# Optimization experiments

Measured on AMD Instinct MI355X. Metric: run time of the kernel, lower is better.

The kernel has to match this reference:

```python
import jax, jax.numpy as jnp
import numpy as np

NA, NF, EA, EF, NG = 200000, 50000, 800000, 200000, 4096
D = 128
BN_EPS = 1e-5

def _bn(x, g, b):
    m = x.mean(axis=0)
    v = x.var(axis=0)
    return g * (x - m) * jax.lax.rsqrt(v + BN_EPS) + b

def _gine(x, src, dst, edge_emb, W1, b1, g1, be1, W2, b2):
    # message = relu(x_src + edge_emb); scatter-add to dst; (1+eps)*x with eps=0
    msg = jax.nn.relu(x[src] + edge_emb)
    agg = jax.ops.segment_sum(msg, dst, num_segments=x.shape[0])
    h = x + agg
    h = jax.nn.relu(_bn(h @ W1 + b1, g1, be1))
    return h @ W2 + b2

def _seg_mean(x, idx, n):
    s = jax.ops.segment_sum(x, idx, num_segments=n)
    c = jax.ops.segment_sum(jnp.ones((x.shape[0],), x.dtype), idx, num_segments=n)
    return s / jnp.maximum(c, 1.0)[:, None]

def setup_inputs() -> dict:
    key = jax.random.key(0)
    ks = jax.random.split(key, 40)
    def nrm(i, shape, scale=0.05):
        return (jax.random.normal(ks[i], shape, dtype=jnp.float32) * scale)
    inp = {
        'atom_x': jax.random.normal(ks[0], (NA, 101), dtype=jnp.float32),
        'fg_x': jax.random.normal(ks[1], (NF, 73), dtype=jnp.float32),
        'atom_edge_attr': jax.random.normal(ks[2], (EA, 11), dtype=jnp.float32),
        'fg_edge_attr': jax.random.normal(ks[3], (EF, 101), dtype=jnp.float32),
        'atom_emb_W': nrm(4, (101, D)), 'atom_emb_b': jnp.zeros((D,), jnp.float32),
        'fg_emb_W': nrm(5, (73, D)), 'fg_emb_b': jnp.zeros((D,), jnp.float32),
        'bond_W': nrm(6, (3, 11, D)), 'bond_b': jnp.zeros((3, D), jnp.float32),
        'ag_W1': nrm(7, (3, D, 2 * D)), 'ag_b1': jnp.zeros((3, 2 * D), jnp.float32),
        'ag_g1': jnp.ones((3, 2 * D), jnp.float32), 'ag_be1': jnp.zeros((3, 2 * D), jnp.float32),
        'ag_W2': nrm(8, (3, 2 * D, D)), 'ag_b2': jnp.zeros((3, D), jnp.float32),
        'abn_g': jnp.ones((3, D), jnp.float32), 'abn_b': jnp.zeros((3, D), jnp.float32),
        'fge_W': nrm(9, (2, 101, D)), 'fge_b': jnp.zeros((2, D), jnp.float32),
        'fg_W1': nrm(10, (2, D, 2 * D)), 'fg_b1': jnp.zeros((2, 2 * D), jnp.float32),
        'fg_g1': jnp.ones((2, 2 * D), jnp.float32), 'fg_be1': jnp.zeros((2, 2 * D), jnp.float32),
        'fg_W2': nrm(11, (2, 2 * D, D)), 'fg_b2': jnp.zeros((2, D), jnp.float32),
        'fbn_g': jnp.ones((2, D), jnp.float32), 'fbn_b': jnp.zeros((2, D), jnp.float32),
        'a2f_W': nrm(12, (D, D)), 'a2f_b': jnp.zeros((D,), jnp.float32),
        'atom_edge_index': jax.random.randint(ks[13], (2, EA), 0, NA, dtype=jnp.int32),
        'fg_edge_index': jax.random.randint(ks[14], (2, EF), 0, NF, dtype=jnp.int32),
        'atom_idx': jax.random.randint(ks[15], (NA,), 0, NA, dtype=jnp.int32),
        'fg_idx': jax.random.randint(ks[16], (NA,), 0, NF, dtype=jnp.int32),
        'fg_batch': jnp.sort(jax.random.randint(ks[17], (NF,), 0, NG, dtype=jnp.int32)),
    }
    return inp

def reference(atom_x, fg_x, atom_edge_attr, fg_edge_attr, atom_emb_W, atom_emb_b, fg_emb_W, fg_emb_b, bond_W, bond_b, ag_W1, ag_b1, ag_g1, ag_be1, ag_W2, ag_b2, abn_g, abn_b, fge_W, fge_b, fg_W1, fg_b1, fg_g1, fg_be1, fg_W2, fg_b2, fbn_g, fbn_b, a2f_W, a2f_b, atom_edge_index, fg_edge_index, atom_idx, fg_idx, fg_batch):
    asrc, adst = atom_edge_index[0], atom_edge_index[1]
    fsrc, fdst = fg_edge_index[0], fg_edge_index[1]
    h = atom_x @ atom_emb_W + atom_emb_b
    for i in range(3):
        eemb = atom_edge_attr @ bond_W[i] + bond_b[i]
        h = _gine(h, asrc, adst, eemb, ag_W1[i], ag_b1[i], ag_g1[i], ag_be1[i], ag_W2[i], ag_b2[i])
        h = _bn(h, abn_g[i], abn_b[i])
        if i != 2:
            h = jax.nn.relu(h)
    a2f = _seg_mean(h[atom_idx], fg_idx, NF) @ a2f_W + a2f_b
    g = fg_x @ fg_emb_W + fg_emb_b + a2f
    for i in range(2):
        eemb = fg_edge_attr @ fge_W[i] + fge_b[i]
        g = _gine(g, fsrc, fdst, eemb, fg_W1[i], fg_b1[i], fg_g1[i], fg_be1[i], fg_W2[i], fg_b2[i])
        g = _bn(g, fbn_g[i], fbn_b[i])
        if i != 1:
            g = jax.nn.relu(g)
    return _seg_mean(g, fg_batch, NG)
```

## Files before the change

### kernel.cpp

```cpp
#include <hip/hip_runtime.h>
#include <cstddef>
#include <cstdint>

#define NA_C 200000
#define NF_C 50000
#define EA_C 800000
#define EF_C 200000
#define NG_C 4096
#define DD 128
#define HH 256
#define SC_CHUNK 2048
#define NPW 8

typedef unsigned short u16;
typedef unsigned int   u32;
typedef float f32x4 __attribute__((ext_vector_type(4)));
typedef short s16x8 __attribute__((ext_vector_type(8)));

__device__ inline float bf2f(u16 h) { return __uint_as_float(((u32)h) << 16); }
__device__ inline u16 f2bf(float f) {
    u32 u = __float_as_uint(f);
    return (u16)((u + 0x7fffu + ((u >> 16) & 1u)) >> 16);
}
__device__ inline float2 up2(u32 u) {
    return make_float2(__uint_as_float(u << 16), __uint_as_float(u & 0xffff0000u));
}
__device__ inline u32 pk2(float x, float y) { return (u32)f2bf(x) | ((u32)f2bf(y) << 16); }

__global__ __launch_bounds__(256) void gemm_b(
    const u16* __restrict__ A, const u16* __restrict__ Bt,
    const float* __restrict__ bias,
    const float* __restrict__ iscale, const float* __restrict__ ishift,
    const u16* __restrict__ Cadd, u16* __restrict__ C,
    int M, int K, int Ntot,
    float* __restrict__ ssum, float* __restrict__ ssq)
{
    __shared__ u16 As[4 * 128 * 8];
    __shared__ u16 Bs[4 * 128 * 8];
    __shared__ float ls[128], lq[128];
    const int tid  = threadIdx.x;
    const int wave = tid >> 6, lane = tid & 63;
    const int quad = lane >> 4, l15 = lane & 15;
    const int wm = (wave & 1) * 64, wn = (wave >> 1) * 64;
    const int m0 = blockIdx.y * 128, n0 = blockIdx.x * 128;
    const int r     = tid >> 1;
    const int cpair = (tid & 1) * 2;

    f32x4 acc[4][4];
#pragma unroll
    for (int i = 0; i < 4; ++i)
#pragma unroll
        for (int j = 0; j < 4; ++j) acc[i][j] = (f32x4)0.f;

    const int m = m0 + r;
    for (int k0 = 0; k0 < K; k0 += 32) {
#pragma unroll
        for (int j = 0; j < 2; ++j) {
            const int cg = cpair + j;
            uint4 av = make_uint4(0, 0, 0, 0);
            if (m < M) av = *(const uint4*)(A + (size_t)m * K + k0 + cg * 8);
            if (iscale) {
                u32* w = (u32*)&av;
#pragma unroll
                for (int q2 = 0; q2 < 4; ++q2) {
                    int kk = k0 + cg * 8 + q2 * 2;
                    float2 f = up2(w[q2]);
                    f.x = fmaxf(fmaf(f.x, iscale[kk],     ishift[kk]),     0.f);
                    f.y = fmaxf(fmaf(f.y, iscale[kk + 1], ishift[kk + 1]), 0.f);
                    w[q2] = pk2(f.x, f.y);
                }
            }
            *(uint4*)&As[(cg * 128 + r) * 8] = av;
        }
#pragma unroll
        for (int j = 0; j < 2; ++j) {
            const int cg = cpair + j;
            uint4 bv = *(const uint4*)(Bt + (size_t)(n0 + r) * K + k0 + cg * 8);
            *(uint4*)&Bs[(cg * 128 + r) * 8] = bv;
        }
        __syncthreads();

        s16x8 a[4], b[4];
#pragma unroll
        for (int mi = 0; mi < 4; ++mi)
            a[mi] = *(const s16x8*)&As[(quad * 128 + wm + mi * 16 + l15) * 8];
#pragma unroll
        for (int ni = 0; ni < 4; ++ni)
            b[ni] = *(const s16x8*)&Bs[(quad * 128 + wn + ni * 16 + l15) * 8];
#pragma unroll
        for (int mi = 0; mi < 4; ++mi)
#pragma unroll
            for (int ni = 0; ni < 4; ++ni)
                acc[mi][ni] = __builtin_amdgcn_mfma_f32_16x16x32_bf16(
                    a[mi], b[ni], acc[mi][ni], 0, 0, 0);
        __syncthreads();
    }

    if (ssum) {
        if (tid < 128) { ls[tid] = 0.f; lq[tid] = 0.f; }
        __syncthreads();
    }

    float cs[4] = {0.f, 0.f, 0.f, 0.f}, cq[4] = {0.f, 0.f, 0.f, 0.f};
#pragma unroll
    for (int mi = 0; mi < 4; ++mi) {
        int rowb = m0 + wm + mi * 16 + quad * 4;
#pragma unroll
        for (int ni = 0; ni < 4; ++ni) {
            int col = n0 + wn + ni * 16 + l15;
            float bv = bias[col];
#pragma unroll
            for (int rr = 0; rr < 4; ++rr) {
                int row = rowb + rr;
                if (row < M) {
                    float v = acc[mi][ni][rr] + bv;
                    size_t idx = (size_t)row * Ntot + col;
                    if (Cadd) v += bf2f(Cadd[idx]);
                    C[idx] = f2bf(v);
                    cs[ni] += v;
                    cq[ni] = fmaf(v, v, cq[ni]);
                }
            }
        }
    }

    if (ssum) {
#pragma unroll
        for (int ni = 0; ni < 4; ++ni) {
            int lc = wn + ni * 16 + l15;
            atomicAdd(&ls[lc], cs[ni]);
            atomicAdd(&lq[lc], cq[ni]);
        }
        __syncthreads();
        if (tid < 128) {
            atomicAdd(&ssum[n0 + tid], ls[tid]);
            atomicAdd(&ssq[n0 + tid], lq[tid]);
        }
    }
}

static inline void gemm_launch(hipStream_t s, const u16* A, const u16* Bt,
    const float* bias, const float* iscale, const float* ishift,
    const u16* Cadd, u16* C, int M, int K, int Ntot,
    float* ssum = nullptr, float* ssq = nullptr)
{
    dim3 grid(Ntot / 128, (M + 127) / 128);
    gemm_b<<<grid, dim3(256), 0, s>>>(A, Bt, bias, iscale, ishift, Cadd, C,
                                      M, K, Ntot, ssum, ssq);
}

__global__ void cvt_pad(const float* __restrict__ src, u32* __restrict__ dst,
                        int M, int K, int Kp2)
{
    int idx = blockIdx.x * 256 + threadIdx.x;
    if (idx >= M * Kp2) return;
    int row = idx / Kp2, c = (idx - row * Kp2) * 2;
    float a = (c < K)     ? src[(size_t)row * K + c]     : 0.f;
    float b = (c + 1 < K) ? src[(size_t)row * K + c + 1] : 0.f;
    dst[idx] = pk2(a, b);
}

__global__ void cvt_pad_perm(const float* __restrict__ src, const int2* __restrict__ csr2,
                             u32* __restrict__ dst, int M, int K, int Kp2)
{
    int idx = blockIdx.x * 256 + threadIdx.x;
    if (idx >= M * Kp2) return;
    int row = idx / Kp2, c = (idx - row * Kp2) * 2;
    int srow = csr2[row].x;
    float a = (c < K)     ? src[(size_t)srow * K + c]     : 0.f;
    float b = (c + 1 < K) ? src[(size_t)srow * K + c + 1] : 0.f;
    dst[idx] = pk2(a, b);
}

__global__ void perm_attr12_k(const float* __restrict__ attr, const int2* __restrict__ csr2,
                              float* __restrict__ out, int ne)
{
    int idx = blockIdx.x * 256 + threadIdx.x;
    if (idx >= ne * 12) return;
    int e = idx / 12, k = idx - e * 12;
    int eid = csr2[e].x;
    out[idx] = (k < 11) ? attr[(size_t)eid * 11 + k] : 0.f;
}

__global__ void prep_wt(const float* __restrict__ W, u16* __restrict__ Wt,
                        int K, int N, int Kp)
{
    int idx = blockIdx.x * 256 + threadIdx.x;
    if (idx >= N * Kp) return;
    int n = idx / Kp, k = idx - n * Kp;
    Wt[idx] = (k < K) ? f2bf(W[(size_t)k * N + n]) : (u16)0;
}

__global__ void hist_k(const int* __restrict__ idx, int n, int* __restrict__ deg)
{
    int i = blockIdx.x * 256 + threadIdx.x;
    if (i < n) atomicAdd(&deg[idx[i]], 1);
}

__global__ __launch_bounds__(256) void scan_part_k(const int* __restrict__ deg, int n,
                                                   int* __restrict__ bsum)
{
    __shared__ int ts[256];
    const int t = threadIdx.x;
    const int base = blockIdx.x * SC_CHUNK + t * 8;
    int s = 0;
#pragma unroll
    for (int j = 0; j < 8; ++j) { int i = base + j; if (i < n) s += deg[i]; }
    ts[t] = s;
    __syncthreads();
    for (int off = 128; off > 0; off >>= 1) {
        if (t < off) ts[t] += ts[t + off];
        __syncthreads();
    }
    if (t == 0) bsum[blockIdx.x] = ts[0];
}

__global__ __launch_bounds__(256) void scan_top_k(int* __restrict__ bsum, int nb)
{
    __shared__ int ss[256];
    const int t = threadIdx.x;
    int v = (t < nb) ? bsum[t] : 0;
    ss[t] = v;
    __syncthreads();
    for (int off = 1; off < 256; off <<= 1) {
        int u = (t >= off) ? ss[t - off] : 0;
        __syncthreads();
        ss[t] += u;
        __syncthreads();
    }
    if (t < nb) bsum[t] = ss[t] - v;
}

__global__ __launch_bounds__(256) void scan_emit_k(const int* __restrict__ deg, int n,
                                                   const int* __restrict__ bsum,
                                                   int* __restrict__ rowptr)
{
    __shared__ int ts[256];
    const int t = threadIdx.x;
    const int base = blockIdx.x * SC_CHUNK + t * 8;
    int d[8], loc[8], s = 0;
#pragma unroll
    for (int j = 0; j < 8; ++j) {
        int i = base + j;
        d[j] = (i < n) ? deg[i] : 0;
        loc[j] = s;
        s += d[j];
    }
    ts[t] = s;
    __syncthreads();
    for (int off = 1; off < 256; off <<= 1) {
        int u = (t >= off) ? ts[t - off] : 0;
        __syncthreads();
        ts[t] += u;
        __syncthreads();
    }
    const int off0 = bsum[blockIdx.x] + (ts[t] - s);
#pragma unroll
    for (int j = 0; j < 8; ++j) {
        int i = base + j;
        if (i < n) {
            rowptr[i] = off0 + loc[j];
            if (i == n - 1) rowptr[n] = off0 + loc[j] + d[j];
        }
    }
}

static void csr_prefix(hipStream_t s, const int* idx, int ne, int nbkt,
                       int* rowptr, int* cursor, int* bsum)
{
    hipMemsetAsync(cursor, 0, (size_t)nbkt * 4, s);
    hist_k<<<(ne + 255) / 256, 256, 0, s>>>(idx, ne, cursor);
    int nblk = (nbkt + SC_CHUNK - 1) / SC_CHUNK;
    scan_part_k<<<nblk, 256, 0, s>>>(cursor, nbkt, bsum);
    scan_top_k<<<1, 256, 0, s>>>(bsum, nblk);
    scan_emit_k<<<nblk, 256, 0, s>>>(cursor, nbkt, bsum, rowptr);
    hipMemcpyAsync(cursor, rowptr, (size_t)nbkt * 4, hipMemcpyDeviceToDevice, s);
}

__global__ void fill2_k(const int* __restrict__ idx, const int* __restrict__ src,
                        int n, int* __restrict__ cursor, int2* __restrict__ csr2)
{
    int i = blockIdx.x * 256 + threadIdx.x;
    if (i < n) {
        int p = atomicAdd(&cursor[idx[i]], 1);
        csr2[p] = make_int2(i, src[i]);
    }
}

__global__ void fillm_k(const int* __restrict__ idx, const int* __restrict__ map,
                        int n, int* __restrict__ cursor, int* __restrict__ csr)
{
    int i = blockIdx.x * 256 + threadIdx.x;
    if (i < n) {
        int p = atomicAdd(&cursor[idx[i]], 1);
        csr[p] = map ? map[i] : i;
    }
}

__global__ __launch_bounds__(256) void gine_agg_atom_b(
    const u32* __restrict__ x2, const float4* __restrict__ attrp,
    const int2* __restrict__ csr2, const int* __restrict__ rowptr,
    const float* __restrict__ Wm, const float* __restrict__ bm,
    const float* __restrict__ tsc, const float* __restrict__ tsh, int trelu,
    u32* __restrict__ out2, int n)
{
    const int lane = threadIdx.x & 63;
    const int v0 = (blockIdx.x * 4 + (threadIdx.x >> 6)) * NPW;
    if (v0 >= n) return;
    const int vend = (v0 + NPW < n) ? v0 + NPW : n;

    const float2 w0 = *(const float2*)&Wm[0 * 128 + 2 * lane];
    const float2 w1 = *(const float2*)&Wm[1 * 128 + 2 * lane];
    const float2 w2 = *(const float2*)&Wm[2 * 128 + 2 * lane];
    const float2 w3 = *(const float2*)&Wm[3 * 128 + 2 * lane];
    const float2 w4 = *(const float2*)&Wm[4 * 128 + 2 * lane];
    const float2 w5 = *(const float2*)&Wm[5 * 128 + 2 * lane];
    const float2 w6 = *(const float2*)&Wm[6 * 128 + 2 * lane];
    const float2 w7 = *(const float2*)&Wm[7 * 128 + 2 * lane];
    const float2 w8 = *(const float2*)&Wm[8 * 128 + 2 * lane];
    const float2 w9 = *(const float2*)&Wm[9 * 128 + 2 * lane];
    const float2 wa = *(const float2*)&Wm[10 * 128 + 2 * lane];
    const float2 bb = *(const float2*)&bm[2 * lane];

    float sc0 = 1.f, sc1 = 1.f, sh0 = 0.f, sh1 = 0.f;
    if (tsc) {
        sc0 = tsc[2 * lane]; sc1 = tsc[2 * lane + 1];
        sh0 = tsh[2 * lane]; sh1 = tsh[2 * lane + 1];
    }

    const int E0 = rowptr[v0], E1 = rowptr[vend];
    int v  = v0;
    int nb = rowptr[v0 + 1];
    u32 xs_n = (v0 + 1 < vend) ? x2[(size_t)(v0 + 1) * 64 + lane] : 0u;
    float2 acc = up2(x2[(size_t)v0 * 64 + lane]);
    acc.x = fmaf(acc.x, sc0, sh0); acc.y = fmaf(acc.y, sc1, sh1);
    if (trelu) { acc.x = fmaxf(acc.x, 0.f); acc.y = fmaxf(acc.y, 0.f); }

    if (E0 < E1) {
        int2 pc = csr2[E0];
        int2 pn = csr2[(E0 + 1 < E1) ? E0 + 1 : E0];
        float4 a0c = attrp[3 * (size_t)E0];
        float4 a1c = attrp[3 * (size_t)E0 + 1];
        float4 a2c = attrp[3 * (size_t)E0 + 2];
        u32 xc = x2[(size_t)pc.y * 64 + lane];
        for (int e = E0; e < E1; ++e) {
            const int en  = (e + 1 < E1) ? e + 1 : e;
            const int en2 = (e + 2 < E1) ? e + 2 : en;
            int2 p2 = csr2[en2];
            u32 xn = x2[(size_t)pn.y * 64 + lane];
            float4 a0n = attrp[3 * (size_t)en];
            float4 a1n = attrp[3 * (size_t)en + 1];
            float4 a2n = attrp[3 * (size_t)en + 2];
            while (e >= nb) {
                out2[(size_t)v * 64 + lane] = pk2(acc.x, acc.y);
                ++v;
                float2 nx = up2(xs_n);
                nx.x = fmaf(nx.x, sc0, sh0); nx.y = fmaf(nx.y, sc1, sh1);
                if (trelu) { nx.x = fmaxf(nx.x, 0.f); nx.y = fmaxf(nx.y, 0.f); }
                acc = nx;
                xs_n = (v + 1 < vend) ? x2[(size_t)(v + 1) * 64 + lane] : xs_n;
                nb = rowptr[v + 1];
            }
            float m0 = bb.x, m1 = bb.y;
            m0 = fmaf(a0c.x, w0.x, m0); m1 = fmaf(a0c.x, w0.y, m1);
            m0 = fmaf(a0c.y, w1.x, m0); m1 = fmaf(a0c.y, w1.y, m1);
            m0 = fmaf(a0c.z, w2.x, m0); m1 = fmaf(a0c.z, w2.y, m1);
            m0 = fmaf(a0c.w, w3.x, m0); m1 = fmaf(a0c.w, w3.y, m1);
            m0 = fmaf(a1c.x, w4.x, m0); m1 = fmaf(a1c.x, w4.y, m1);
            m0 = fmaf(a1c.y, w5.x, m0); m1 = fmaf(a1c.y, w5.y, m1);
            m0 = fmaf(a1c.z, w6.x, m0); m1 = fmaf(a1c.z, w6.y, m1);
            m0 = fmaf(a1c.w, w7.x, m0); m1 = fmaf(a1c.w, w7.y, m1);
            m0 = fmaf(a2c.x, w8.x, m0); m1 = fmaf(a2c.x, w8.y, m1);
            m0 = fmaf(a2c.y, w9.x, m0); m1 = fmaf(a2c.y, w9.y, m1);
            m0 = fmaf(a2c.z, wa.x, m0); m1 = fmaf(a2c.z, wa.y, m1);
            float2 s = up2(xc);
            s.x = fmaf(s.x, sc0, sh0); s.y = fmaf(s.y, sc1, sh1);
            if (trelu) { s.x = fmaxf(s.x, 0.f); s.y = fmaxf(s.y, 0.f); }
            acc.x += fmaxf(s.x + m0, 0.f);
            acc.y += fmaxf(s.y + m1, 0.f);
            pn = p2; xc = xn;
            a0c = a0n; a1c = a1n; a2c = a2n;
        }
    }
    for (;;) {
        out2[(size_t)v * 64 + lane] = pk2(acc.x, acc.y);
        ++v;
        if (v >= vend) break;
        float2 nx = up2(xs_n);
        nx.x = fmaf(nx.x, sc0, sh0); nx.y = fmaf(nx.y, sc1, sh1);
        if (trelu) { nx.x = fmaxf(nx.x, 0.f); nx.y = fmaxf(nx.y, 0.f); }
        acc = nx;
        xs_n = (v + 1 < vend) ? x2[(size_t)(v + 1) * 64 + lane] : xs_n;
    }
}

__global__ __launch_bounds__(256) void gine_agg_pre_b(
    const u32* __restrict__ x2, const u32* __restrict__ eemb2,
    const int2* __restrict__ csr2, const int* __restrict__ rowptr,
    const float* __restrict__ tsc, const float* __restrict__ tsh, int trelu,
    u32* __restrict__ out2, int n)
{
    const int lane = threadIdx.x & 63;
    const int v0 = (blockIdx.x * 4 + (threadIdx.x >> 6)) * NPW;
    if (v0 >= n) return;
    const int vend = (v0 + NPW < n) ? v0 + NPW : n;

    float sc0 = 1.f, sc1 = 1.f, sh0 = 0.f, sh1 = 0.f;
    if (tsc) {
        sc0 = tsc[2 * lane]; sc1 = tsc[2 * lane + 1];
        sh0 = tsh[2 * lane]; sh1 = tsh[2 * lane + 1];
    }

    const int E0 = rowptr[v0], E1 = rowptr[vend];
    int v  = v0;
    int nb = rowptr[v0 + 1];
    u32 xs_n = (v0 + 1 < vend) ? x2[(size_t)(v0 + 1) * 64 + lane] : 0u;
    float2 acc = up2(x2[(size_t)v0 * 64 + lane]);
    acc.x = fmaf(acc.x, sc0, sh0); acc.y = fmaf(acc.y, sc1, sh1);
    if (trelu) { acc.x = fmaxf(acc.x, 0.f); acc.y = fmaxf(acc.y, 0.f); }

    if (E0 < E1) {
        int2 pc = csr2[E0];
        int2 pn = csr2[(E0 + 1 < E1) ? E0 + 1 : E0];
        u32 xc = x2[(size_t)pc.y * 64 + lane];
        u32 mc = eemb2[(size_t)E0 * 64 + lane];
        for (int e = E0; e < E1; ++e) {
            const int en  = (e + 1 < E1) ? e + 1 : e;
            const int en2 = (e + 2 < E1) ? e + 2 : en;
            int2 p2 = csr2[en2];
            u32 xn = x2[(size_t)pn.y * 64 + lane];
            u32 mn = eemb2[(size_t)en * 64 + lane];
            while (e >= nb) {
                out2[(size_t)v * 64 + lane] = pk2(acc.x, acc.y);
                ++v;
                float2 nx = up2(xs_n);
                nx.x = fmaf(nx.x, sc0, sh0); nx.y = fmaf(nx.y, sc1, sh1);
                if (trelu) { nx.x = fmaxf(nx.x, 0.f); nx.y = fmaxf(nx.y, 0.f); }
                acc = nx;
                xs_n = (v + 1 < vend) ? x2[(size_t)(v + 1) * 64 + lane] : xs_n;
                nb = rowptr[v + 1];
            }
            float2 m = up2(mc);
            float2 s = up2(xc);
            s.x = fmaf(s.x, sc0, sh0); s.y = fmaf(s.y, sc1, sh1);
            if (trelu) { s.x = fmaxf(s.x, 0.f); s.y = fmaxf(s.y, 0.f); }
            acc.x += fmaxf(m.x + s.x, 0.f);
            acc.y += fmaxf(m.y + s.y, 0.f);
            pn = p2; xc = xn; mc = mn;
        }
    }
    for (;;) {
        out2[(size_t)v * 64 + lane] = pk2(acc.x, acc.y);
        ++v;
        if (v >= vend) break;
        float2 nx = up2(xs_n);
        nx.x = fmaf(nx.x, sc0, sh0); nx.y = fmaf(nx.y, sc1, sh1);
        if (trelu) { nx.x = fmaxf(nx.x, 0.f); nx.y = fmaxf(nx.y, 0.f); }
        acc = nx;
        xs_n = (v + 1 < vend) ? x2[(size_t)(v + 1) * 64 + lane] : xs_n;
    }
}

__global__ __launch_bounds__(256) void seg_mean_b2b(
    const u32* __restrict__ x2, const int* __restrict__ csr,
    const int* __restrict__ rowptr,
    const float* __restrict__ tsc, const float* __restrict__ tsh,
    u32* __restrict__ out2, int n)
{
    const int lane = threadIdx.x & 63;
    const int v = blockIdx.x * 4 + (threadIdx.x >> 6);
    if (v >= n) return;
    const int e0 = rowptr[v], e1 = rowptr[v + 1];
    float2 acc = make_float2(0.f, 0.f);
    if (e0 < e1) {
        int cc = csr[e0];
        int cn = csr[(e0 + 1 < e1) ? e0 + 1 : e0];
        u32 xc = x2[(size_t)cc * 64 + lane];
        for (int e = e0; e < e1; ++e) {
            const int en  = (e + 1 < e1) ? e + 1 : e;
            const int en2 = (e + 2 < e1) ? e + 2 : en;
            int c2 = csr[en2];
            u32 xn = x2[(size_t)cn * 64 + lane];
            float2 s = up2(xc);
            acc.x += s.x; acc.y += s.y;
            cn = c2; xc = xn;
        }
    }
    float inv = 1.f / fmaxf((float)(e1 - e0), 1.f);
    float2 r = make_float2(acc.x * inv, acc.y * inv);
    if (tsc) {
        if (e1 > e0) {
            r.x = fmaf(r.x, tsc[2 * lane],     tsh[2 * lane]);
            r.y = fmaf(r.y, tsc[2 * lane + 1], tsh[2 * lane + 1]);
        } else {
            r.x = 0.f; r.y = 0.f;
        }
    }
    out2[(size_t)v * 64 + lane] = pk2(r.x, r.y);
}

__global__ __launch_bounds__(256) void seg_mean_b2f(
    const u32* __restrict__ x2, const int* __restrict__ csr,
    const int* __restrict__ rowptr,
    const float* __restrict__ tsc, const float* __restrict__ tsh,
    float* __restrict__ out, int n)
{
    const int lane = threadIdx.x & 63;
    const int v = blockIdx.x * 4 + (threadIdx.x >> 6);
    if (v >= n) return;
    const int e0 = rowptr[v], e1 = rowptr[v + 1];
    float2 acc = make_float2(0.f, 0.f);
    if (e0 < e1) {
        int cc = csr[e0];
        int cn = csr[(e0 + 1 < e1) ? e0 + 1 : e0];
        u32 xc = x2[(size_t)cc * 64 + lane];
        for (int e = e0; e < e1; ++e) {
            const int en  = (e + 1 < e1) ? e + 1 : e;
            const int en2 = (e + 2 < e1) ? e + 2 : en;
            int c2 = csr[en2];
            u32 xn = x2[(size_t)cn * 64 + lane];
            float2 s = up2(xc);
            acc.x += s.x; acc.y += s.y;
            cn = c2; xc = xn;
        }
    }
    float inv = 1.f / fmaxf((float)(e1 - e0), 1.f);
    float2 r = make_float2(acc.x * inv, acc.y * inv);
    if (tsc) {
        if (e1 > e0) {
            r.x = fmaf(r.x, tsc[2 * lane],     tsh[2 * lane]);
            r.y = fmaf(r.y, tsc[2 * lane + 1], tsh[2 * lane + 1]);
        } else {
            r.x = 0.f; r.y = 0.f;
        }
    }
    *(float2*)&out[(size_t)v * 128 + lane * 2] = r;
}

__global__ void bn_finalize(const float* __restrict__ sum, const float* __restrict__ sumsq,
                            const float* __restrict__ g, const float* __restrict__ be,
                            float minv, float* __restrict__ sc, float* __restrict__ sh, int N)
{
    int c = threadIdx.x;
    if (c < N) {
        float m = sum[c] * minv;
        float v = fmaxf(sumsq[c] * minv - m * m, 0.f);
        float s = g[c] * rsqrtf(v + 1e-5f);
        sc[c] = s;
        sh[c] = fmaf(-m, s, be[c]);
    }
}

extern "C" void kernel_launch(void* const* d_in, const int* in_sizes, int n_in,
                              void* d_out, int out_size, void* d_ws, size_t ws_size,
                              hipStream_t stream)
{
    const float* atom_x        = (const float*)d_in[0];
    const float* fg_x          = (const float*)d_in[1];
    const float* atom_edge_attr= (const float*)d_in[2];
    const float* fg_edge_attr  = (const float*)d_in[3];
    const float* atom_emb_W    = (const float*)d_in[4];
    const float* atom_emb_b    = (const float*)d_in[5];
    const float* fg_emb_W      = (const float*)d_in[6];
    const float* fg_emb_b      = (const float*)d_in[7];
    const float* bond_W        = (const float*)d_in[8];
    const float* bond_b        = (const float*)d_in[9];
    const float* ag_W1         = (const float*)d_in[10];
    const float* ag_b1         = (const float*)d_in[11];
    const float* ag_g1         = (const float*)d_in[12];
    const float* ag_be1        = (const float*)d_in[13];
    const float* ag_W2         = (const float*)d_in[14];
    const float* ag_b2         = (const float*)d_in[15];
    const float* abn_g         = (const float*)d_in[16];
    const float* abn_b         = (const float*)d_in[17];
    const float* fge_W         = (const float*)d_in[18];
    const float* fge_b         = (const float*)d_in[19];
    const float* fg_W1         = (const float*)d_in[20];
    const float* fg_b1         = (const float*)d_in[21];
    const float* fg_g1         = (const float*)d_in[22];
    const float* fg_be1        = (const float*)d_in[23];
    const float* fg_W2         = (const float*)d_in[24];
    const float* fg_b2         = (const float*)d_in[25];
    const float* fbn_g         = (const float*)d_in[26];
    const float* fbn_b         = (const float*)d_in[27];
    const float* a2f_W         = (const float*)d_in[28];
    const float* a2f_b         = (const float*)d_in[29];
    const int*   aei           = (const int*)d_in[30];
    const int*   fei           = (const int*)d_in[31];
    const int*   atom_idx      = (const int*)d_in[32];
    const int*   fg_idx        = (const int*)d_in[33];
    const int*   fg_batch      = (const int*)d_in[34];
    const int *asrc = aei, *adst = aei + EA_C;
    const int *fsrc = fei, *fdst = fei + EF_C;

    char* base = (char*)d_ws;
    const size_t SZ_H = (size_t)NA_C * DD * 2;
    u16* hA = (u16*)base;
    u16* hB = (u16*)(base + SZ_H);
    u16* TB = (u16*)(base + 2 * SZ_H);
    u16* XB = (u16*)(base + 2 * SZ_H + (size_t)NA_C * HH * 2);
    char* csrb = (char*)XB + SZ_H;
    int*  aR  = (int*)csrb;
    int*  aCu = aR + (NA_C + 2);
    int*  bS  = aCu + NA_C;
    int2* aE2 = (int2*)(bS + 258);
    char* wtb = (char*)(aE2 + EA_C);
    wtb = (char*)(((uintptr_t)wtb + 15) & ~(uintptr_t)15);
    u16* WT_aemb = (u16*)wtb;                 wtb += 128 * 128 * 2;
    u16* WT_aW1  = (u16*)wtb;                 wtb += 3 * 256 * 128 * 2;
    u16* WT_aW2  = (u16*)wtb;                 wtb += 3 * 128 * 256 * 2;
    u16* WT_a2f  = (u16*)wtb;                 wtb += 128 * 128 * 2;
    u16* WT_femb = (u16*)wtb;                 wtb += 128 * 96 * 2;
    u16* WT_fge  = (u16*)wtb;                 wtb += 2 * 128 * 128 * 2;
    u16* WT_fW1  = (u16*)wtb;                 wtb += 2 * 256 * 128 * 2;
    u16* WT_fW2  = (u16*)wtb;                 wtb += 2 * 128 * 256 * 2;
    float* stats = (float*)wtb;               wtb += 10240 * sizeof(float);
    float* S_SUM = stats;
    float* S_SQ  = stats + 2560;
    float* S_SC  = stats + 5120;
    float* S_SH  = stats + 7680;

    {
        int g = (128 * 128 + 255) / 256;
        prep_wt<<<g, 256, 0, stream>>>(atom_emb_W, WT_aemb, 101, 128, 128);
        prep_wt<<<g, 256, 0, stream>>>(a2f_W, WT_a2f, 128, 128, 128);
        for (int i = 0; i < 3; ++i) {
            prep_wt<<<(256 * 128 + 255) / 256, 256, 0, stream>>>(
                ag_W1 + (size_t)i * 128 * 256, WT_aW1 + (size_t)i * 256 * 128, 128, 256, 128);
            prep_wt<<<(128 * 256 + 255) / 256, 256, 0, stream>>>(
                ag_W2 + (size_t)i * 256 * 128, WT_aW2 + (size_t)i * 128 * 256, 256, 128, 256);
        }
        prep_wt<<<(128 * 96 + 255) / 256, 256, 0, stream>>>(fg_emb_W, WT_femb, 73, 128, 96);
        for (int i = 0; i < 2; ++i) {
            prep_wt<<<g, 256, 0, stream>>>(
                fge_W + (size_t)i * 101 * 128, WT_fge + (size_t)i * 128 * 128, 101, 128, 128);
            prep_wt<<<(256 * 128 + 255) / 256, 256, 0, stream>>>(
                fg_W1 + (size_t)i * 128 * 256, WT_fW1 + (size_t)i * 256 * 128, 128, 256, 128);
            prep_wt<<<(128 * 256 + 255) / 256, 256, 0, stream>>>(
                fg_W2 + (size_t)i * 256 * 128, WT_fW2 + (size_t)i * 128 * 256, 256, 128, 256);
        }
    }
    hipMemsetAsync(stats, 0, 5120 * sizeof(float), stream);

    csr_prefix(stream, adst, EA_C, NA_C, aR, aCu, bS);
    fill2_k<<<(EA_C + 255) / 256, 256, 0, stream>>>(adst, asrc, EA_C, aCu, aE2);

    cvt_pad<<<((size_t)NA_C * 64 + 255) / 256, 256, 0, stream>>>(atom_x, (u32*)XB, NA_C, 101, 64);

    gemm_launch(stream, XB, WT_aemb, atom_emb_b, nullptr, nullptr, nullptr, hA, NA_C, 128, 128);

    float* attrP = (float*)XB;
    perm_attr12_k<<<((size_t)EA_C * 12 + 255) / 256, 256, 0, stream>>>(
        atom_edge_attr, aE2, attrP, EA_C);

    const int agrid = (NA_C + 4 * NPW - 1) / (4 * NPW);
    u16* hc = hA;
    const float* cur_sc = nullptr;
    const float* cur_sh = nullptr;
    int cur_relu = 0;
    for (int i = 0; i < 3; ++i) {
        u16* hn = (hc == hA) ? hB : hA;
        const int st1 = 2 * i, st2 = 2 * i + 1;
        gine_agg_atom_b<<<agrid, 256, 0, stream>>>(
            (const u32*)hc, (const float4*)attrP, aE2, aR,
            bond_W + (size_t)i * 11 * DD, bond_b + i * DD,
            cur_sc, cur_sh, cur_relu, (u32*)hn, NA_C);
        gemm_launch(stream, hn, WT_aW1 + (size_t)i * 256 * 128,
                    ag_b1 + i * HH, nullptr, nullptr, nullptr, TB, NA_C, 128, HH,
                    S_SUM + st1 * 256, S_SQ + st1 * 256);
        bn_finalize<<<1, HH, 0, stream>>>(S_SUM + st1 * 256, S_SQ + st1 * 256,
                                          ag_g1 + i * HH, ag_be1 + i * HH,
                                          1.f / NA_C, S_SC + st1 * 256, S_SH + st1 * 256, HH);
        gemm_launch(stream, TB, WT_aW2 + (size_t)i * 128 * 256,
                    ag_b2 + i * DD, S_SC + st1 * 256, S_SH + st1 * 256, nullptr, hn,
                    NA_C, 256, 128,
                    S_SUM + st2 * 256, S_SQ + st2 * 256);
        bn_finalize<<<1, DD, 0, stream>>>(S_SUM + st2 * 256, S_SQ + st2 * 256,
                                          abn_g + i * DD, abn_b + i * DD,
                                          1.f / NA_C, S_SC + st2 * 256, S_SH + st2 * 256, DD);
        cur_sc = S_SC + st2 * 256; cur_sh = S_SH + st2 * 256; cur_relu = (i != 2);
        hc = hn;
    }

    {
        int* xE = (int*)aE2;
        csr_prefix(stream, fg_idx, NA_C, NF_C, aR, aCu, bS);
        fillm_k<<<(NA_C + 255) / 256, 256, 0, stream>>>(fg_idx, atom_idx, NA_C, aCu, xE);
        seg_mean_b2b<<<(NF_C + 3) / 4, 256, 0, stream>>>(
            (const u32*)hc, xE, aR, cur_sc, cur_sh, (u32*)hA, NF_C);
    }
    u16* means   = hA;
    u16* a2f_lin = hA + (size_t)NF_C * DD;
    gemm_launch(stream, means, WT_a2f, a2f_b, nullptr, nullptr, nullptr, a2f_lin, NF_C, 128, 128);

    u16* fgx_bf = hA + (size_t)NF_C * DD * 2;
    cvt_pad<<<((size_t)NF_C * 48 + 255) / 256, 256, 0, stream>>>(fg_x, (u32*)fgx_bf, NF_C, 73, 48);
    u16* g = hB;
    gemm_launch(stream, fgx_bf, WT_femb, fg_emb_b, nullptr, nullptr, a2f_lin, g, NF_C, 96, 128);

    csr_prefix(stream, fdst, EF_C, NF_C, aR, aCu, bS);
    fill2_k<<<(EF_C + 255) / 256, 256, 0, stream>>>(fdst, fsrc, EF_C, aCu, aE2);
    cvt_pad_perm<<<((size_t)EF_C * 64 + 255) / 256, 256, 0, stream>>>(
        fg_edge_attr, aE2, (u32*)XB, EF_C, 101, 64);

    const int fgrid = (NF_C + 4 * NPW - 1) / (4 * NPW);
    u16* eemb = TB;
    u16* gn   = hA + (size_t)NF_C * DD * 2 + (size_t)NF_C * 96;
    u16* gt   = TB + (size_t)EF_C * DD;
    const float* gsc = nullptr;
    const float* gsh = nullptr;
    int grelu = 0;
    for (int i = 0; i < 2; ++i) {
        const int st1 = 6 + 2 * i, st2 = 7 + 2 * i;
        gemm_launch(stream, XB, WT_fge + (size_t)i * 128 * 128,
                    fge_b + i * DD, nullptr, nullptr, nullptr, eemb, EF_C, 128, 128);
        gine_agg_pre_b<<<fgrid, 256, 0, stream>>>(
            (const u32*)g, (const u32*)eemb, aE2, aR, gsc, gsh, grelu, (u32*)gn, NF_C);
        gemm_launch(stream, gn, WT_fW1 + (size_t)i * 256 * 128,
                    fg_b1 + i * HH, nullptr, nullptr, nullptr, gt, NF_C, 128, HH,
                    S_SUM + st1 * 256, S_SQ + st1 * 256);
        bn_finalize<<<1, HH, 0, stream>>>(S_SUM + st1 * 256, S_SQ + st1 * 256,
                                          fg_g1 + i * HH, fg_be1 + i * HH,
                                          1.f / NF_C, S_SC + st1 * 256, S_SH + st1 * 256, HH);
        gemm_launch(stream, gt, WT_fW2 + (size_t)i * 128 * 256,
                    fg_b2 + i * DD, S_SC + st1 * 256, S_SH + st1 * 256, nullptr, g,
                    NF_C, 256, 128,
                    S_SUM + st2 * 256, S_SQ + st2 * 256);
        bn_finalize<<<1, DD, 0, stream>>>(S_SUM + st2 * 256, S_SQ + st2 * 256,
                                          fbn_g + i * DD, fbn_b + i * DD,
                                          1.f / NF_C, S_SC + st2 * 256, S_SH + st2 * 256, DD);
        gsc = S_SC + st2 * 256; gsh = S_SH + st2 * 256; grelu = (i != 1);
    }

    {
        int* bR  = (int*)(gt + (size_t)NF_C * HH);
        int* bCu = bR + (NG_C + 1);
        int* bE  = bCu + NG_C;
        csr_prefix(stream, fg_batch, NF_C, NG_C, bR, bCu, bS);
        fillm_k<<<(NF_C + 255) / 256, 256, 0, stream>>>(fg_batch, nullptr, NF_C, bCu, bE);
        seg_mean_b2f<<<(NG_C + 3) / 4, 256, 0, stream>>>(
            (const u32*)g, bE, bR, gsc, gsh, (float*)d_out, NG_C);
    }
}
```

Before: 2.173 ms.

## Fuse BN finalize into consumers, batch weight prep, use direct-to-LDS GEMM loads

Removes the standalone bn_finalize kernels. Each consumer (GEMM prologue, aggregation kernels, segment-mean kernels) now computes the BN scale and shift from the raw sum and sum-of-squares buffers. The fifteen prep_wt launches become a single job-table kernel, which cuts per-launch overhead. The GEMM's unscaled A path and its B loads now use global_load_lds to copy 16 bytes straight into LDS instead of staging through registers. The A path drops the row bounds check, so the last partial tile reads past M rows, which relies on the buffer extending that far.

```diff
diff --git a/kernel.cpp b/kernel.cpp
--- a/kernel.cpp
+++ b/kernel.cpp
@@ -27,10 +27,17 @@
 }
 __device__ inline u32 pk2(float x, float y) { return (u32)f2bf(x) | ((u32)f2bf(y) << 16); }
 
+__device__ inline void gll16(const void* g, void* l) {
+    __builtin_amdgcn_global_load_lds(
+        (const __attribute__((address_space(1))) void*)g,
+        (__attribute__((address_space(3))) void*)l, 16, 0, 0);
+}
+
 __global__ __launch_bounds__(256) void gemm_b(
     const u16* __restrict__ A, const u16* __restrict__ Bt,
     const float* __restrict__ bias,
-    const float* __restrict__ iscale, const float* __restrict__ ishift,
+    const float* __restrict__ isum, const float* __restrict__ isq,
+    const float* __restrict__ ig, const float* __restrict__ ibe, float iminv,
     const u16* __restrict__ Cadd, u16* __restrict__ C,
     int M, int K, int Ntot,
     float* __restrict__ ssum, float* __restrict__ ssq)
@@ -38,6 +45,7 @@
     __shared__ u16 As[4 * 128 * 8];
     __shared__ u16 Bs[4 * 128 * 8];
     __shared__ float ls[128], lq[128];
+    __shared__ float sIsc[256], sIsh[256];
     const int tid  = threadIdx.x;
     const int wave = tid >> 6, lane = tid & 63;
     const int quad = lane >> 4, l15 = lane & 15;
@@ -46,6 +54,17 @@
     const int r     = tid >> 1;
     const int cpair = (tid & 1) * 2;
 
+    if (isum) {
+        if (tid < K) {
+            float mu = isum[tid] * iminv;
+            float va = fmaxf(isq[tid] * iminv - mu * mu, 0.f);
+            float s  = ig[tid] * rsqrtf(va + 1e-5f);
+            sIsc[tid] = s;
+            sIsh[tid] = fmaf(-mu, s, ibe[tid]);
+        }
+        __syncthreads();
+    }
+
     f32x4 acc[4][4];
 #pragma unroll
     for (int i = 0; i < 4; ++i)
@@ -54,29 +73,34 @@
 
     const int m = m0 + r;
     for (int k0 = 0; k0 < K; k0 += 32) {
-#pragma unroll
-        for (int j = 0; j < 2; ++j) {
-            const int cg = cpair + j;
-            uint4 av = make_uint4(0, 0, 0, 0);
-            if (m < M) av = *(const uint4*)(A + (size_t)m * K + k0 + cg * 8);
-            if (iscale) {
+        if (isum) {
+#pragma unroll
+            for (int j = 0; j < 2; ++j) {
+                const int cg = cpair + j;
+                uint4 av = make_uint4(0, 0, 0, 0);
+                if (m < M) av = *(const uint4*)(A + (size_t)m * K + k0 + cg * 8);
                 u32* w = (u32*)&av;
 #pragma unroll
                 for (int q2 = 0; q2 < 4; ++q2) {
                     int kk = k0 + cg * 8 + q2 * 2;
                     float2 f = up2(w[q2]);
-                    f.x = fmaxf(fmaf(f.x, iscale[kk],     ishift[kk]),     0.f);
-                    f.y = fmaxf(fmaf(f.y, iscale[kk + 1], ishift[kk + 1]), 0.f);
+                    f.x = fmaxf(fmaf(f.x, sIsc[kk],     sIsh[kk]),     0.f);
+                    f.y = fmaxf(fmaf(f.y, sIsc[kk + 1], sIsh[kk + 1]), 0.f);
                     w[q2] = pk2(f.x, f.y);
                 }
+                *(uint4*)&As[(cg * 128 + r) * 8] = av;
             }
-            *(uint4*)&As[(cg * 128 + r) * 8] = av;
+        } else {
+#pragma unroll
+            for (int j = 0; j < 2; ++j) {
+                gll16(A + (size_t)(m0 + j * 64 + lane) * K + k0 + wave * 8,
+                      &As[(wave * 128 + j * 64) * 8]);
+            }
         }
 #pragma unroll
         for (int j = 0; j < 2; ++j) {
-            const int cg = cpair + j;
-            uint4 bv = *(const uint4*)(Bt + (size_t)(n0 + r) * K + k0 + cg * 8);
-            *(uint4*)&Bs[(cg * 128 + r) * 8] = bv;
+            gll16(Bt + (size_t)(n0 + j * 64 + lane) * K + k0 + wave * 8,
+                  &Bs[(wave * 128 + j * 64) * 8]);
         }
         __syncthreads();
 
@@ -140,13 +164,14 @@
 }
 
 static inline void gemm_launch(hipStream_t s, const u16* A, const u16* Bt,
-    const float* bias, const float* iscale, const float* ishift,
-    const u16* Cadd, u16* C, int M, int K, int Ntot,
+    const float* bias,
+    const float* isum, const float* isq, const float* ig, const float* ibe,
+    float iminv, const u16* Cadd, u16* C, int M, int K, int Ntot,
     float* ssum = nullptr, float* ssq = nullptr)
 {
     dim3 grid(Ntot / 128, (M + 127) / 128);
-    gemm_b<<<grid, dim3(256), 0, s>>>(A, Bt, bias, iscale, ishift, Cadd, C,
-                                      M, K, Ntot, ssum, ssq);
+    gemm_b<<<grid, dim3(256), 0, s>>>(A, Bt, bias, isum, isq, ig, ibe, iminv,
+                                      Cadd, C, M, K, Ntot, ssum, ssq);
 }
 
 __global__ void cvt_pad(const float* __restrict__ src, u32* __restrict__ dst,
@@ -182,13 +207,25 @@
     out[idx] = (k < 11) ? attr[(size_t)eid * 11 + k] : 0.f;
 }
 
-__global__ void prep_wt(const float* __restrict__ W, u16* __restrict__ Wt,
-                        int K, int N, int Kp)
+#define NJOBS 15
+struct WtJobs {
+    const float* W[NJOBS];
+    u16* Wt[NJOBS];
+    int K[NJOBS], N[NJOBS], Kp[NJOBS], end[NJOBS];
+};
+
+__global__ void prep_wt_all(WtJobs jobs, int total)
 {
     int idx = blockIdx.x * 256 + threadIdx.x;
-    if (idx >= N * Kp) return;
-    int n = idx / Kp, k = idx - n * Kp;
-    Wt[idx] = (k < K) ? f2bf(W[(size_t)k * N + n]) : (u16)0;
+    if (idx >= total) return;
+    int j = 0;
+    while (idx >= jobs.end[j]) ++j;
+    int base = j ? jobs.end[j - 1] : 0;
+    int loc = idx - base;
+    int Kp = jobs.Kp[j];
+    int n = loc / Kp, k = loc - n * Kp;
+    jobs.Wt[j][loc] = (k < jobs.K[j])
+        ? f2bf(jobs.W[j][(size_t)k * jobs.N[j] + n]) : (u16)0;
 }
 
 __global__ void hist_k(const int* __restrict__ idx, int n, int* __restrict__ deg)
@@ -297,11 +334,26 @@
     }
 }
 
+__device__ inline void bn_lane(const float* bsum, const float* bsq,
+                               const float* bg, const float* bbe, float minv,
+                               int lane, float& sc0, float& sc1, float& sh0, float& sh1)
+{
+    float mu0 = bsum[2 * lane] * minv,     mu1 = bsum[2 * lane + 1] * minv;
+    float va0 = fmaxf(bsq[2 * lane] * minv - mu0 * mu0, 0.f);
+    float va1 = fmaxf(bsq[2 * lane + 1] * minv - mu1 * mu1, 0.f);
+    sc0 = bg[2 * lane] * rsqrtf(va0 + 1e-5f);
+    sc1 = bg[2 * lane + 1] * rsqrtf(va1 + 1e-5f);
+    sh0 = fmaf(-mu0, sc0, bbe[2 * lane]);
+    sh1 = fmaf(-mu1, sc1, bbe[2 * lane + 1]);
+}
+
 __global__ __launch_bounds__(256) void gine_agg_atom_b(
     const u32* __restrict__ x2, const float4* __restrict__ attrp,
     const int2* __restrict__ csr2, const int* __restrict__ rowptr,
     const float* __restrict__ Wm, const float* __restrict__ bm,
-    const float* __restrict__ tsc, const float* __restrict__ tsh, int trelu,
+    const float* __restrict__ bsum, const float* __restrict__ bsq,
+    const float* __restrict__ bg, const float* __restrict__ bbe,
+    float bminv, int trelu,
     u32* __restrict__ out2, int n)
 {
     const int lane = threadIdx.x & 63;
@@ -323,10 +375,7 @@
     const float2 bb = *(const float2*)&bm[2 * lane];
 
     float sc0 = 1.f, sc1 = 1.f, sh0 = 0.f, sh1 = 0.f;
-    if (tsc) {
-        sc0 = tsc[2 * lane]; sc1 = tsc[2 * lane + 1];
-        sh0 = tsh[2 * lane]; sh1 = tsh[2 * lane + 1];
-    }
+    if (bsum) bn_lane(bsum, bsq, bg, bbe, bminv, lane, sc0, sc1, sh0, sh1);
 
     const int E0 = rowptr[v0], E1 = rowptr[vend];
     int v  = v0;
@@ -397,7 +446,9 @@
 __global__ __launch_bounds__(256) void gine_agg_pre_b(
     const u32* __restrict__ x2, const u32* __restrict__ eemb2,
     const int2* __restrict__ csr2, const int* __restrict__ rowptr,
-    const float* __restrict__ tsc, const float* __restrict__ tsh, int trelu,
+    const float* __restrict__ bsum, const float* __restrict__ bsq,
+    const float* __restrict__ bg, const float* __restrict__ bbe,
+    float bminv, int trelu,
     u32* __restrict__ out2, int n)
 {
     const int lane = threadIdx.x & 63;
@@ -406,10 +457,7 @@
     const int vend = (v0 + NPW < n) ? v0 + NPW : n;
 
     float sc0 = 1.f, sc1 = 1.f, sh0 = 0.f, sh1 = 0.f;
-    if (tsc) {
-        sc0 = tsc[2 * lane]; sc1 = tsc[2 * lane + 1];
-        sh0 = tsh[2 * lane]; sh1 = tsh[2 * lane + 1];
-    }
+    if (bsum) bn_lane(bsum, bsq, bg, bbe, bminv, lane, sc0, sc1, sh0, sh1);
 
     const int E0 = rowptr[v0], E1 = rowptr[vend];
     int v  = v0;
@@ -464,7 +512,8 @@
 __global__ __launch_bounds__(256) void seg_mean_b2b(
     const u32* __restrict__ x2, const int* __restrict__ csr,
     const int* __restrict__ rowptr,
-    const float* __restrict__ tsc, const float* __restrict__ tsh,
+    const float* __restrict__ bsum, const float* __restrict__ bsq,
+    const float* __restrict__ bg, const float* __restrict__ bbe, float bminv,
     u32* __restrict__ out2, int n)
 {
     const int lane = threadIdx.x & 63;
@@ -488,10 +537,12 @@
     }
     float inv = 1.f / fmaxf((float)(e1 - e0), 1.f);
     float2 r = make_float2(acc.x * inv, acc.y * inv);
-    if (tsc) {
+    if (bsum) {
         if (e1 > e0) {
-            r.x = fmaf(r.x, tsc[2 * lane],     tsh[2 * lane]);
-            r.y = fmaf(r.y, tsc[2 * lane + 1], tsh[2 * lane + 1]);
+            float sc0, sc1, sh0, sh1;
+            bn_lane(bsum, bsq, bg, bbe, bminv, lane, sc0, sc1, sh0, sh1);
+            r.x = fmaf(r.x, sc0, sh0);
+            r.y = fmaf(r.y, sc1, sh1);
         } else {
             r.x = 0.f; r.y = 0.f;
         }
@@ -502,7 +553,8 @@
 __global__ __launch_bounds__(256) void seg_mean_b2f(
     const u32* __restrict__ x2, const int* __restrict__ csr,
     const int* __restrict__ rowptr,
-    const float* __restrict__ tsc, const float* __restrict__ tsh,
+    const float* __restrict__ bsum, const float* __restrict__ bsq,
+    const float* __restrict__ bg, const float* __restrict__ bbe, float bminv,
     float* __restrict__ out, int n)
 {
     const int lane = threadIdx.x & 63;
@@ -526,29 +578,17 @@
     }
     float inv = 1.f / fmaxf((float)(e1 - e0), 1.f);
     float2 r = make_float2(acc.x * inv, acc.y * inv);
-    if (tsc) {
+    if (bsum) {
         if (e1 > e0) {
-            r.x = fmaf(r.x, tsc[2 * lane],     tsh[2 * lane]);
-            r.y = fmaf(r.y, tsc[2 * lane + 1], tsh[2 * lane + 1]);
+            float sc0, sc1, sh0, sh1;
+            bn_lane(bsum, bsq, bg, bbe, bminv, lane, sc0, sc1, sh0, sh1);
+            r.x = fmaf(r.x, sc0, sh0);
+            r.y = fmaf(r.y, sc1, sh1);
         } else {
             r.x = 0.f; r.y = 0.f;
         }
     }
     *(float2*)&out[(size_t)v * 128 + lane * 2] = r;
-}
-
-__global__ void bn_finalize(const float* __restrict__ sum, const float* __restrict__ sumsq,
-                            const float* __restrict__ g, const float* __restrict__ be,
-                            float minv, float* __restrict__ sc, float* __restrict__ sh, int N)
-{
-    int c = threadIdx.x;
-    if (c < N) {
-        float m = sum[c] * minv;
-        float v = fmaxf(sumsq[c] * minv - m * m, 0.f);
-        float s = g[c] * rsqrtf(v + 1e-5f);
-        sc[c] = s;
-        sh[c] = fmaf(-m, s, be[c]);
-    }
 }
 
 extern "C" void kernel_launch(void* const* d_in, const int* in_sizes, int n_in,
@@ -614,31 +654,31 @@
     u16* WT_fge  = (u16*)wtb;                 wtb += 2 * 128 * 128 * 2;
     u16* WT_fW1  = (u16*)wtb;                 wtb += 2 * 256 * 128 * 2;
     u16* WT_fW2  = (u16*)wtb;                 wtb += 2 * 128 * 256 * 2;
-    float* stats = (float*)wtb;               wtb += 10240 * sizeof(float);
+    float* stats = (float*)wtb;               wtb += 5120 * sizeof(float);
     float* S_SUM = stats;
     float* S_SQ  = stats + 2560;
-    float* S_SC  = stats + 5120;
-    float* S_SH  = stats + 7680;
 
     {
-        int g = (128 * 128 + 255) / 256;
-        prep_wt<<<g, 256, 0, stream>>>(atom_emb_W, WT_aemb, 101, 128, 128);
-        prep_wt<<<g, 256, 0, stream>>>(a2f_W, WT_a2f, 128, 128, 128);
-        for (int i = 0; i < 3; ++i) {
-            prep_wt<<<(256 * 128 + 255) / 256, 256, 0, stream>>>(
-                ag_W1 + (size_t)i * 128 * 256, WT_aW1 + (size_t)i * 256 * 128, 128, 256, 128);
-            prep_wt<<<(128 * 256 + 255) / 256, 256, 0, stream>>>(
-                ag_W2 + (size_t)i * 256 * 128, WT_aW2 + (size_t)i * 128 * 256, 256, 128, 256);
-        }
-        prep_wt<<<(128 * 96 + 255) / 256, 256, 0, stream>>>(fg_emb_W, WT_femb, 73, 128, 96);
-        for (int i = 0; i < 2; ++i) {
-            prep_wt<<<g, 256, 0, stream>>>(
-                fge_W + (size_t)i * 101 * 128, WT_fge + (size_t)i * 128 * 128, 101, 128, 128);
-            prep_wt<<<(256 * 128 + 255) / 256, 256, 0, stream>>>(
-                fg_W1 + (size_t)i * 128 * 256, WT_fW1 + (size_t)i * 256 * 128, 128, 256, 128);
-            prep_wt<<<(128 * 256 + 255) / 256, 256, 0, stream>>>(
-                fg_W2 + (size_t)i * 256 * 128, WT_fW2 + (size_t)i * 128 * 256, 256, 128, 256);
-        }
+        WtJobs jb;
+        int t = 0, acc = 0;
+        auto add = [&](const float* W, u16* Wt, int K, int N, int Kp) {
+            jb.W[t] = W; jb.Wt[t] = Wt; jb.K[t] = K; jb.N[t] = N; jb.Kp[t] = Kp;
+            acc += N * Kp; jb.end[t] = acc; ++t;
+        };
+        add(atom_emb_W, WT_aemb, 101, 128, 128);
+        add(a2f_W,      WT_a2f,  128, 128, 128);
+        for (int i = 0; i < 3; ++i)
+            add(ag_W1 + (size_t)i * 128 * 256, WT_aW1 + (size_t)i * 256 * 128, 128, 256, 128);
+        for (int i = 0; i < 3; ++i)
+            add(ag_W2 + (size_t)i * 256 * 128, WT_aW2 + (size_t)i * 128 * 256, 256, 128, 256);
+        add(fg_emb_W,   WT_femb, 73, 128, 96);
+        for (int i = 0; i < 2; ++i)
+            add(fge_W + (size_t)i * 101 * 128, WT_fge + (size_t)i * 128 * 128, 101, 128, 128);
+        for (int i = 0; i < 2; ++i)
+            add(fg_W1 + (size_t)i * 128 * 256, WT_fW1 + (size_t)i * 256 * 128, 128, 256, 128);
+        for (int i = 0; i < 2; ++i)
+            add(fg_W2 + (size_t)i * 256 * 128, WT_fW2 + (size_t)i * 128 * 256, 256, 128, 256);
+        prep_wt_all<<<(acc + 255) / 256, 256, 0, stream>>>(jb, acc);
     }
     hipMemsetAsync(stats, 0, 5120 * sizeof(float), stream);
 
@@ -647,7 +687,8 @@
 
     cvt_pad<<<((size_t)NA_C * 64 + 255) / 256, 256, 0, stream>>>(atom_x, (u32*)XB, NA_C, 101, 64);
 
-    gemm_launch(stream, XB, WT_aemb, atom_emb_b, nullptr, nullptr, nullptr, hA, NA_C, 128, 128);
+    gemm_launch(stream, XB, WT_aemb, atom_emb_b,
+                nullptr, nullptr, nullptr, nullptr, 0.f, nullptr, hA, NA_C, 128, 128);
 
     float* attrP = (float*)XB;
     perm_attr12_k<<<((size_t)EA_C * 12 + 255) / 256, 256, 0, stream>>>(
@@ -655,8 +696,8 @@
 
     const int agrid = (NA_C + 4 * NPW - 1) / (4 * NPW);
     u16* hc = hA;
-    const float* cur_sc = nullptr;
-    const float* cur_sh = nullptr;
+    const float* cb_sum = nullptr; const float* cb_sq = nullptr;
+    const float* cb_g = nullptr;   const float* cb_be = nullptr;
     int cur_relu = 0;
     for (int i = 0; i < 3; ++i) {
         u16* hn = (hc == hA) ? hB : hA;
@@ -664,21 +705,20 @@
         gine_agg_atom_b<<<agrid, 256, 0, stream>>>(
             (const u32*)hc, (const float4*)attrP, aE2, aR,
             bond_W + (size_t)i * 11 * DD, bond_b + i * DD,
-            cur_sc, cur_sh, cur_relu, (u32*)hn, NA_C);
+            cb_sum, cb_sq, cb_g, cb_be, 1.f / NA_C, cur_relu, (u32*)hn, NA_C);
         gemm_launch(stream, hn, WT_aW1 + (size_t)i * 256 * 128,
-                    ag_b1 + i * HH, nullptr, nullptr, nullptr, TB, NA_C, 128, HH,
+                    ag_b1 + i * HH, nullptr, nullptr, nullptr, nullptr, 0.f,
+                    nullptr, TB, NA_C, 128, HH,
                     S_SUM + st1 * 256, S_SQ + st1 * 256);
-        bn_finalize<<<1, HH, 0, stream>>>(S_SUM + st1 * 256, S_SQ + st1 * 256,
-                                          ag_g1 + i * HH, ag_be1 + i * HH,
-                                          1.f / NA_C, S_SC + st1 * 256, S_SH + st1 * 256, HH);
         gemm_launch(stream, TB, WT_aW2 + (size_t)i * 128 * 256,
-                    ag_b2 + i * DD, S_SC + st1 * 256, S_SH + st1 * 256, nullptr, hn,
-                    NA_C, 256, 128,
+                    ag_b2 + i * DD,
+                    S_SUM + st1 * 256, S_SQ + st1 * 256,
+                    ag_g1 + i * HH, ag_be1 + i * HH, 1.f / NA_C,
+                    nullptr, hn, NA_C, 256, 128,
                     S_SUM + st2 * 256, S_SQ + st2 * 256);
-        bn_finalize<<<1, DD, 0, stream>>>(S_SUM + st2 * 256, S_SQ + st2 * 256,
-                                          abn_g + i * DD, abn_b + i * DD,
-                                          1.f / NA_C, S_SC + st2 * 256, S_SH + st2 * 256, DD);
-        cur_sc = S_SC + st2 * 256; cur_sh = S_SH + st2 * 256; cur_relu = (i != 2);
+        cb_sum = S_SUM + st2 * 256; cb_sq = S_SQ + st2 * 256;
+        cb_g = abn_g + i * DD; cb_be = abn_b + i * DD;
+        cur_relu = (i != 2);
         hc = hn;
     }
 
@@ -687,16 +727,19 @@
         csr_prefix(stream, fg_idx, NA_C, NF_C, aR, aCu, bS);
         fillm_k<<<(NA_C + 255) / 256, 256, 0, stream>>>(fg_idx, atom_idx, NA_C, aCu, xE);
         seg_mean_b2b<<<(NF_C + 3) / 4, 256, 0, stream>>>(
-            (const u32*)hc, xE, aR, cur_sc, cur_sh, (u32*)hA, NF_C);
+            (const u32*)hc, xE, aR, cb_sum, cb_sq, cb_g, cb_be, 1.f / NA_C,
+            (u32*)hA, NF_C);
     }
     u16* means   = hA;
     u16* a2f_lin = hA + (size_t)NF_C * DD;
-    gemm_launch(stream, means, WT_a2f, a2f_b, nullptr, nullptr, nullptr, a2f_lin, NF_C, 128, 128);
+    gemm_launch(stream, means, WT_a2f, a2f_b,
+                nullptr, nullptr, nullptr, nullptr, 0.f, nullptr, a2f_lin, NF_C, 128, 128);
 
     u16* fgx_bf = hA + (size_t)NF_C * DD * 2;
     cvt_pad<<<((size_t)NF_C * 48 + 255) / 256, 256, 0, stream>>>(fg_x, (u32*)fgx_bf, NF_C, 73, 48);
     u16* g = hB;
-    gemm_launch(stream, fgx_bf, WT_femb, fg_emb_b, nullptr, nullptr, a2f_lin, g, NF_C, 96, 128);
+    gemm_launch(stream, fgx_bf, WT_femb, fg_emb_b,
+                nullptr, nullptr, nullptr, nullptr, 0.f, a2f_lin, g, NF_C, 96, 128);
 
     csr_prefix(stream, fdst, EF_C, NF_C, aR, aCu, bS);
     fill2_k<<<(EF_C + 255) / 256, 256, 0, stream>>>(fdst, fsrc, EF_C, aCu, aE2);
@@ -707,29 +750,30 @@
     u16* eemb = TB;
     u16* gn   = hA + (size_t)NF_C * DD * 2 + (size_t)NF_C * 96;
     u16* gt   = TB + (size_t)EF_C * DD;
-    const float* gsc = nullptr;
-    const float* gsh = nullptr;
+    const float* gb_sum = nullptr; const float* gb_sq = nullptr;
+    const float* gb_g = nullptr;   const float* gb_be = nullptr;
     int grelu = 0;
     for (int i = 0; i < 2; ++i) {
         const int st1 = 6 + 2 * i, st2 = 7 + 2 * i;
         gemm_launch(stream, XB, WT_fge + (size_t)i * 128 * 128,
-                    fge_b + i * DD, nullptr, nullptr, nullptr, eemb, EF_C, 128, 128);
+                    fge_b + i * DD, nullptr, nullptr, nullptr, nullptr, 0.f,
+                    nullptr, eemb, EF_C, 128, 128);
         gine_agg_pre_b<<<fgrid, 256, 0, stream>>>(
-            (const u32*)g, (const u32*)eemb, aE2, aR, gsc, gsh, grelu, (u32*)gn, NF_C);
+            (const u32*)g, (const u32*)eemb, aE2, aR,
+            gb_sum, gb_sq, gb_g, gb_be, 1.f / NF_C, grelu, (u32*)gn, NF_C);
         gemm_launch(stream, gn, WT_fW1 + (size_t)i * 256 * 128,
-                    fg_b1 + i * HH, nullptr, nullptr, nullptr, gt, NF_C, 128, HH,
+                    fg_b1 + i * HH, nullptr, nullptr, nullptr, nullptr, 0.f,
+                    nullptr, gt, NF_C, 128, HH,
                     S_SUM + st1 * 256, S_SQ + st1 * 256);
-        bn_finalize<<<1, HH, 0, stream>>>(S_SUM + st1 * 256, S_SQ + st1 * 256,
-                                          fg_g1 + i * HH, fg_be1 + i * HH,
-                                          1.f / NF_C, S_SC + st1 * 256, S_SH + st1 * 256, HH);
         gemm_launch(stream, gt, WT_fW2 + (size_t)i * 128 * 256,
-                    fg_b2 + i * DD, S_SC + st1 * 256, S_SH + st1 * 256, nullptr, g,
-                    NF_C, 256, 128,
+                    fg_b2 + i * DD,
+                    S_SUM + st1 * 256, S_SQ + st1 * 256,
+                    fg_g1 + i * HH, fg_be1 + i * HH, 1.f / NF_C,
+                    nullptr, g, NF_C, 256, 128,
                     S_SUM + st2 * 256, S_SQ + st2 * 256);
-        bn_finalize<<<1, DD, 0, stream>>>(S_SUM + st2 * 256, S_SQ + st2 * 256,
-                                          fbn_g + i * DD, fbn_b + i * DD,
-                                          1.f / NF_C, S_SC + st2 * 256, S_SH + st2 * 256, DD);
-        gsc = S_SC + st2 * 256; gsh = S_SH + st2 * 256; grelu = (i != 1);
+        gb_sum = S_SUM + st2 * 256; gb_sq = S_SQ + st2 * 256;
+        gb_g = fbn_g + i * DD; gb_be = fbn_b + i * DD;
+        grelu = (i != 1);
     }
 
     {
@@ -739,6 +783,7 @@
         csr_prefix(stream, fg_batch, NF_C, NG_C, bR, bCu, bS);
         fillm_k<<<(NF_C + 255) / 256, 256, 0, stream>>>(fg_batch, nullptr, NF_C, bCu, bE);
         seg_mean_b2f<<<(NG_C + 3) / 4, 256, 0, stream>>>(
-            (const u32*)g, bE, bR, gsc, gsh, (float*)d_out, NG_C);
-    }
-}
+            (const u32*)g, bE, bR, gb_sum, gb_sq, gb_g, gb_be, 1.f / NF_C,
+            (float*)d_out, NG_C);
+    }
+}
```

Measured after the change: 2.129 ms. -2.0%, faster.
